# Kernel optimization log

Measured on AMD Instinct MI355X. Metric: run time of the kernel, lower is better.

## Reference

```python
import jax, jax.numpy as jnp
import numpy as np
from jax import lax

SR = 4096.0        # sample_rate_Hz
N_LAYERS = 4
N_STATE = 64       # state_dim
E = 2              # d_inner (expand=2, d_model=1)
K = 4              # depthwise conv kernel
DT_RANK = 1
B, L = 32, 4096


def setup_inputs() -> dict:
    key = jax.random.key(0)
    ks = jax.random.split(key, 10)
    s = 0.02
    x = jax.random.normal(ks[0], (B, L), dtype=jnp.float32)
    W_in   = jax.random.normal(ks[1], (N_LAYERS, 1, 2 * E), jnp.float32) * 1.0
    conv_w = jax.random.normal(ks[2], (N_LAYERS, E, K), jnp.float32) * 0.5
    conv_b = jnp.zeros((N_LAYERS, E), jnp.float32)
    W_x    = jax.random.normal(ks[3], (N_LAYERS, E, DT_RANK + 2 * N_STATE), jnp.float32) * s
    W_dt   = jax.random.normal(ks[4], (N_LAYERS, DT_RANK, E), jnp.float32) * s
    b_dt   = jnp.zeros((N_LAYERS, E), jnp.float32)
    # S4D-real style init: A = -exp(A_log), A_log = log(1..N)
    A_log  = jnp.broadcast_to(jnp.log(jnp.arange(1, N_STATE + 1, dtype=jnp.float32)), (N_LAYERS, E, N_STATE)).copy()
    D_skip = jnp.ones((N_LAYERS, E), jnp.float32)
    W_out  = jax.random.normal(ks[5], (N_LAYERS, E, 1), jnp.float32) * s
    return {"x": x, "W_in": W_in, "conv_w": conv_w, "conv_b": conv_b, "W_x": W_x,
            "W_dt": W_dt, "b_dt": b_dt, "A_log": A_log, "D_skip": D_skip, "W_out": W_out}


def _causal_dwconv(u, w, b):
    # u: [B,L,E], w: [E,K] depthwise causal conv
    Klen = w.shape[1]
    up = jnp.pad(u, ((0, 0), (Klen - 1, 0), (0, 0)))
    y = sum(up[:, k:k + u.shape[1], :] * w[None, None, :, k] for k in range(Klen))
    return y + b


def _selective_scan(u, delta, A, Bm, Cm, Dv):
    # u,delta: [B,L,E]; A: [E,N]; Bm,Cm: [B,L,N]; Dv: [E]
    dA = jnp.exp(delta[..., None] * A)                       # [B,L,E,N]
    dBu = delta[..., None] * Bm[:, :, None, :] * u[..., None]  # [B,L,E,N]

    def step(h, inp):
        dA_t, dBu_t, C_t = inp                               # [B,E,N],[B,E,N],[B,N]
        h = dA_t * h + dBu_t
        y = jnp.einsum('ben,bn->be', h, C_t)
        return h, y

    h0 = jnp.zeros((u.shape[0],) + A.shape, dtype=u.dtype)
    _, ys = lax.scan(step, h0, (dA.transpose(1, 0, 2, 3), dBu.transpose(1, 0, 2, 3), Cm.transpose(1, 0, 2)))
    return ys.transpose(1, 0, 2) + u * Dv                    # [B,L,E]


def _mamba_block(x, W_in, conv_w, conv_b, W_x, W_dt, b_dt, A_log, D_skip, W_out):
    # x: [B,L,1]
    xz = x @ W_in                                            # [B,L,2E]
    u, z = xz[..., :E], xz[..., E:]
    u = jax.nn.silu(_causal_dwconv(u, conv_w, conv_b))       # [B,L,E]
    proj = u @ W_x                                           # [B,L,DT_RANK+2N]
    dt = proj[..., :DT_RANK]
    Bm = proj[..., DT_RANK:DT_RANK + N_STATE]
    Cm = proj[..., DT_RANK + N_STATE:]
    delta = jax.nn.softplus(dt @ W_dt + b_dt) / SR           # [B,L,E], timestep tied to sample rate
    A = -jnp.exp(A_log)                                      # [E,N]
    y = _selective_scan(u, delta, A, Bm, Cm, D_skip)
    y = y * jax.nn.silu(z)
    return y @ W_out + x                                     # residual, [B,L,1]


def reference(x, W_in, conv_w, conv_b, W_x, W_dt, b_dt, A_log, D_skip, W_out):
    h = x[..., None]                                         # [B,L,1]
    for i in range(N_LAYERS):
        h = _mamba_block(h, W_in[i], conv_w[i], conv_b[i], W_x[i], W_dt[i],
                         b_dt[i], A_log[i], D_skip[i], W_out[i])
    return h[..., 0]
```

## Files before the change

### kernel.cpp

```cpp
#include <hip/hip_runtime.h>
#include <hip/hip_bf16.h>


constexpr int   Bsz = 32;
constexpr int   Lsz = 4096;
constexpr int   NC  = 64;
constexpr int   CL  = 64;
constexpr float SRinv = 1.0f / 4096.0f;

__device__ __forceinline__ float sigmoidf_(float v) {
    return 1.0f / (1.0f + __expf(-v));
}

__global__ __launch_bounds__(128) void k_chunk_scan(
    const float* __restrict__ xin,
    const float* __restrict__ W_in,
    const float* __restrict__ conv_w,
    const float* __restrict__ conv_b,
    const float* __restrict__ W_x,
    const float* __restrict__ W_dt,
    const float* __restrict__ b_dt,
    const float* __restrict__ A_log,
    float4* __restrict__ ud,
    float*  __restrict__ Pc,
    float*  __restrict__ Sc)
{
    const int c = blockIdx.x, b = blockIdx.y, tid = threadIdx.x;
    __shared__ float  xs[CL + 3];
    __shared__ float4 s_ud[CL];
    const int base = b * Lsz + c * CL;

    if (tid < CL + 3) {
        int l = c * CL + tid - 3;
        xs[tid] = (l >= 0) ? xin[b * Lsz + l] : 0.0f;
    }
    __syncthreads();

    if (tid < CL) {
        const int t = tid;
        float x0 = xs[t], x1 = xs[t + 1], x2 = xs[t + 2], x3 = xs[t + 3];
        float u[2];
        #pragma unroll
        for (int e = 0; e < 2; e++) {
            float v = W_in[e] * (x0 * conv_w[e * 4 + 0] + x1 * conv_w[e * 4 + 1] +
                                 x2 * conv_w[e * 4 + 2] + x3 * conv_w[e * 4 + 3]) +
                      conv_b[e];
            u[e] = v * sigmoidf_(v);
        }
        float dt = u[0] * W_x[0] + u[1] * W_x[129];
        float dl[2];
        #pragma unroll
        for (int e = 0; e < 2; e++) {
            float a = dt * W_dt[e] + b_dt[e];
            float sp = (a > 20.0f) ? a : log1pf(__expf(a));
            dl[e] = sp * SRinv;
        }
        float4 v4 = make_float4(u[0], u[1], dl[0], dl[1]);
        s_ud[t] = v4;
        ud[base + t] = v4;
    }
    __syncthreads();

    const int e = tid >> 6, n = tid & 63;
    const float Aen = -__expf(A_log[e * 64 + n]);
    const float wb0 = W_x[1 + n], wb1 = W_x[129 + 1 + n];
    float P = 1.0f, S = 0.0f;
    #pragma unroll 8
    for (int l = 0; l < CL; l++) {
        float4 v = s_ud[l];
        float ue = e ? v.y : v.x;
        float d  = e ? v.w : v.z;
        float Bn = v.x * wb0 + v.y * wb1;
        float dA = __expf(d * Aen);
        S = dA * S + (d * ue) * Bn;
        P *= dA;
    }
    const int idx = (b * NC + c) * 128 + tid;
    Pc[idx] = P;
    Sc[idx] = S;
}

__global__ __launch_bounds__(128) void k_output(
    const float* __restrict__ xin,
    const float4* __restrict__ ud,
    const float* __restrict__ Pc,
    const float* __restrict__ Sc,
    const float* __restrict__ W_in,
    const float* __restrict__ W_x,
    const float* __restrict__ A_log,
    const float* __restrict__ D_skip,
    const float* __restrict__ W_out,
    float* __restrict__ out)
{
    const int c = blockIdx.x, b = blockIdx.y, tid = threadIdx.x;
    constexpr int T = 32;
    __shared__ float4 s_ud[CL];
    __shared__ float  xs[CL];
    __shared__ float  ps[T * 2 * 65];
    __shared__ float  ys[T * 2];
    const int base = b * Lsz + c * CL;

    if (tid < CL) {
        s_ud[tid] = ud[base + tid];
        xs[tid]   = xin[base + tid];
    }

    const int e = tid >> 6, n = tid & 63;
    const float Aen = -__expf(A_log[e * 64 + n]);
    const float wb0 = W_x[1 + n],  wb1 = W_x[129 + 1 + n];
    const float wc0 = W_x[65 + n], wc1 = W_x[129 + 65 + n];
    const float wz0 = W_in[2], wz1 = W_in[3];
    const float D0 = D_skip[0], D1 = D_skip[1];
    const float wo0 = W_out[0], wo1 = W_out[1];

    float h = 0.0f;
    if (c > 0) {
        const float* Pb = Pc + (size_t)b * NC * 128 + tid;
        const float* Sb = Sc + (size_t)b * NC * 128 + tid;
        float runS = 0.0f, runP = 1.0f;
        #pragma unroll 8
        for (int j = c - 1; j >= 0; --j) {
            float Sj = Sb[j * 128];
            float Pj = Pb[j * 128];
            runS = __fmaf_rn(runP, Sj, runS);
            runP *= Pj;
        }
        h = runS;
    }
    __syncthreads();

    for (int tile = 0; tile < CL / T; tile++) {
        #pragma unroll 8
        for (int t = 0; t < T; t++) {
            float4 v = s_ud[tile * T + t];
            float ue = e ? v.y : v.x;
            float d  = e ? v.w : v.z;
            float Bn = v.x * wb0 + v.y * wb1;
            float Cn = v.x * wc0 + v.y * wc1;
            float dA = __expf(d * Aen);
            h = dA * h + (d * ue) * Bn;
            ps[(t * 2 + e) * 65 + n] = h * Cn;
        }
        __syncthreads();
        if (tid < T * 2) {
            const int r = tid, t = r >> 1, re = r & 1;
            const float* row = &ps[r * 65];
            float a0 = 0, a1 = 0, a2 = 0, a3 = 0;
            #pragma unroll
            for (int j = 0; j < 64; j += 4) {
                a0 += row[j]; a1 += row[j + 1]; a2 += row[j + 2]; a3 += row[j + 3];
            }
            float4 v = s_ud[tile * T + t];
            float ue = re ? v.y : v.x;
            ys[r] = (a0 + a1) + (a2 + a3) + ue * (re ? D1 : D0);
        }
        __syncthreads();
        if (tid < T) {
            int l = tile * T + tid;
            float y0 = ys[tid * 2], y1 = ys[tid * 2 + 1];
            float xv = xs[l];
            float z0 = xv * wz0, z1 = xv * wz1;
            out[base + l] = y0 * (z0 * sigmoidf_(z0)) * wo0 +
                            y1 * (z1 * sigmoidf_(z1)) * wo1 + xv;
        }
        __syncthreads();
    }
}

extern "C" void kernel_launch(void* const* d_in, const int* in_sizes, int n_in,
                              void* d_out, int out_size, void* d_ws, size_t ws_size,
                              hipStream_t stream) {
    const float* x      = (const float*)d_in[0];
    const float* W_in   = (const float*)d_in[1];
    const float* conv_w = (const float*)d_in[2];
    const float* conv_b = (const float*)d_in[3];
    const float* W_x    = (const float*)d_in[4];
    const float* W_dt   = (const float*)d_in[5];
    const float* b_dt   = (const float*)d_in[6];
    const float* A_log  = (const float*)d_in[7];
    const float* D_skip = (const float*)d_in[8];
    const float* W_out  = (const float*)d_in[9];
    float* out = (float*)d_out;

    float* ws   = (float*)d_ws;
    float4* ud  = (float4*)ws;
    float* Pc   = ws + (size_t)Bsz * Lsz * 4;
    float* Sc   = Pc + (size_t)Bsz * NC * 128;
    float* buf0 = Sc + (size_t)Bsz * NC * 128;
    float* buf1 = buf0 + (size_t)Bsz * Lsz;

    const float* cur = x;
    for (int i = 0; i < 4; i++) {
        float* o = (i == 3) ? out : ((i & 1) ? buf1 : buf0);
        k_chunk_scan<<<dim3(NC, Bsz), 128, 0, stream>>>(
            cur, W_in + i * 4, conv_w + i * 8, conv_b + i * 2,
            W_x + i * 258, W_dt + i * 2, b_dt + i * 2, A_log + i * 128,
            ud, Pc, Sc);
        k_output<<<dim3(NC, Bsz), 128, 0, stream>>>(
            cur, ud, Pc, Sc, W_in + i * 4, W_x + i * 258,
            A_log + i * 128, D_skip + i * 2, W_out + i * 2, o);
        cur = o;
    }
}
```

Measured before the change: 171.6 us.

## Use one 64-thread wave per chunk, each thread scanning both channels with float2

Both kernels drop from 128 to 64 threads per block. Each thread now handles one state index n for both inner channels at once, using two-wide float vectors, and the per-chunk P/S carries are stored as float2 pairs. This shares the B/C projection and the ud loads across the two channels, and it lets all 64 threads do the row reduction and the final output instead of idle subsets. The cost is half as many threads in flight and a longer dependent chain per thread, which may reduce latency hiding. The output kernel also reads ud straight from global memory rather than staging it in LDS.

New measurement: 166.8 us. 1.03x faster.

```diff
diff --git a/kernel.cpp b/kernel.cpp
--- a/kernel.cpp
+++ b/kernel.cpp
@@ -1,5 +1,4 @@
 #include <hip/hip_runtime.h>
-#include <hip/hip_bf16.h>
 
 
 constexpr int   Bsz = 32;
@@ -8,11 +7,13 @@
 constexpr int   CL  = 64;
 constexpr float SRinv = 1.0f / 4096.0f;
 
+typedef float fx2 __attribute__((ext_vector_type(2)));
+
 __device__ __forceinline__ float sigmoidf_(float v) {
     return 1.0f / (1.0f + __expf(-v));
 }
 
-__global__ __launch_bounds__(128) void k_chunk_scan(
+__global__ __launch_bounds__(64) void k_chunk_scan(
     const float* __restrict__ xin,
     const float* __restrict__ W_in,
     const float* __restrict__ conv_w,
@@ -22,23 +23,20 @@
     const float* __restrict__ b_dt,
     const float* __restrict__ A_log,
     float4* __restrict__ ud,
-    float*  __restrict__ Pc,
-    float*  __restrict__ Sc)
+    fx2* __restrict__ Pc,
+    fx2* __restrict__ Sc)
 {
-    const int c = blockIdx.x, b = blockIdx.y, tid = threadIdx.x;
+    const int c = blockIdx.x, b = blockIdx.y, n = threadIdx.x;
     __shared__ float  xs[CL + 3];
     __shared__ float4 s_ud[CL];
     const int base = b * Lsz + c * CL;
 
-    if (tid < CL + 3) {
-        int l = c * CL + tid - 3;
-        xs[tid] = (l >= 0) ? xin[b * Lsz + l] : 0.0f;
-    }
+    xs[3 + n] = xin[base + n];
+    if (n < 3) xs[n] = (c > 0) ? xin[base - 3 + n] : 0.0f;
     __syncthreads();
 
-    if (tid < CL) {
-        const int t = tid;
-        float x0 = xs[t], x1 = xs[t + 1], x2 = xs[t + 2], x3 = xs[t + 3];
+    {
+        float x0 = xs[n], x1 = xs[n + 1], x2 = xs[n + 2], x3 = xs[n + 3];
         float u[2];
         #pragma unroll
         for (int e = 0; e < 2; e++) {
@@ -56,35 +54,35 @@
             dl[e] = sp * SRinv;
         }
         float4 v4 = make_float4(u[0], u[1], dl[0], dl[1]);
-        s_ud[t] = v4;
-        ud[base + t] = v4;
+        s_ud[n] = v4;
+        ud[base + n] = v4;
     }
     __syncthreads();
 
-    const int e = tid >> 6, n = tid & 63;
-    const float Aen = -__expf(A_log[e * 64 + n]);
+    const fx2 A2 = { -__expf(A_log[n]), -__expf(A_log[64 + n]) };
     const float wb0 = W_x[1 + n], wb1 = W_x[129 + 1 + n];
-    float P = 1.0f, S = 0.0f;
+    fx2 P = {1.0f, 1.0f}, S = {0.0f, 0.0f};
     #pragma unroll 8
     for (int l = 0; l < CL; l++) {
         float4 v = s_ud[l];
-        float ue = e ? v.y : v.x;
-        float d  = e ? v.w : v.z;
         float Bn = v.x * wb0 + v.y * wb1;
-        float dA = __expf(d * Aen);
-        S = dA * S + (d * ue) * Bn;
+        fx2 u = {v.x, v.y};
+        fx2 d = {v.z, v.w};
+        fx2 darg = d * A2;
+        fx2 dA = { __expf(darg.x), __expf(darg.y) };
+        S = dA * S + (d * u) * Bn;
         P *= dA;
     }
-    const int idx = (b * NC + c) * 128 + tid;
+    const int idx = (b * NC + c) * 64 + n;
     Pc[idx] = P;
     Sc[idx] = S;
 }
 
-__global__ __launch_bounds__(128) void k_output(
+__global__ __launch_bounds__(64) void k_output(
     const float* __restrict__ xin,
     const float4* __restrict__ ud,
-    const float* __restrict__ Pc,
-    const float* __restrict__ Sc,
+    const fx2* __restrict__ Pc,
+    const fx2* __restrict__ Sc,
     const float* __restrict__ W_in,
     const float* __restrict__ W_x,
     const float* __restrict__ A_log,
@@ -92,78 +90,72 @@
     const float* __restrict__ W_out,
     float* __restrict__ out)
 {
-    const int c = blockIdx.x, b = blockIdx.y, tid = threadIdx.x;
+    const int c = blockIdx.x, b = blockIdx.y, n = threadIdx.x;
     constexpr int T = 32;
-    __shared__ float4 s_ud[CL];
-    __shared__ float  xs[CL];
-    __shared__ float  ps[T * 2 * 65];
-    __shared__ float  ys[T * 2];
+    __shared__ float ps[2 * T][65];
+    __shared__ float ys[2 * CL];
     const int base = b * Lsz + c * CL;
 
-    if (tid < CL) {
-        s_ud[tid] = ud[base + tid];
-        xs[tid]   = xin[base + tid];
-    }
-
-    const int e = tid >> 6, n = tid & 63;
-    const float Aen = -__expf(A_log[e * 64 + n]);
+    const fx2 A2 = { -__expf(A_log[n]), -__expf(A_log[64 + n]) };
     const float wb0 = W_x[1 + n],  wb1 = W_x[129 + 1 + n];
     const float wc0 = W_x[65 + n], wc1 = W_x[129 + 65 + n];
-    const float wz0 = W_in[2], wz1 = W_in[3];
-    const float D0 = D_skip[0], D1 = D_skip[1];
-    const float wo0 = W_out[0], wo1 = W_out[1];
 
-    float h = 0.0f;
+    fx2 h = {0.0f, 0.0f};
     if (c > 0) {
-        const float* Pb = Pc + (size_t)b * NC * 128 + tid;
-        const float* Sb = Sc + (size_t)b * NC * 128 + tid;
-        float runS = 0.0f, runP = 1.0f;
+        const fx2* Pb = Pc + (size_t)b * NC * 64 + n;
+        const fx2* Sb = Sc + (size_t)b * NC * 64 + n;
+        fx2 runS = {0.0f, 0.0f}, runP = {1.0f, 1.0f};
         #pragma unroll 8
         for (int j = c - 1; j >= 0; --j) {
-            float Sj = Sb[j * 128];
-            float Pj = Pb[j * 128];
-            runS = __fmaf_rn(runP, Sj, runS);
+            fx2 Sj = Sb[j * 64];
+            fx2 Pj = Pb[j * 64];
+            runS = runP * Sj + runS;
             runP *= Pj;
         }
         h = runS;
     }
-    __syncthreads();
 
-    for (int tile = 0; tile < CL / T; tile++) {
+    for (int tile = 0; tile < CL / T; ++tile) {
         #pragma unroll 8
-        for (int t = 0; t < T; t++) {
-            float4 v = s_ud[tile * T + t];
-            float ue = e ? v.y : v.x;
-            float d  = e ? v.w : v.z;
+        for (int q = 0; q < T; q++) {
+            float4 v = ud[base + tile * T + q];
             float Bn = v.x * wb0 + v.y * wb1;
             float Cn = v.x * wc0 + v.y * wc1;
-            float dA = __expf(d * Aen);
-            h = dA * h + (d * ue) * Bn;
-            ps[(t * 2 + e) * 65 + n] = h * Cn;
+            fx2 u = {v.x, v.y};
+            fx2 d = {v.z, v.w};
+            fx2 darg = d * A2;
+            fx2 dA = { __expf(darg.x), __expf(darg.y) };
+            h = dA * h + (d * u) * Bn;
+            fx2 yc = h * Cn;
+            ps[q * 2 + 0][n] = yc.x;
+            ps[q * 2 + 1][n] = yc.y;
         }
         __syncthreads();
-        if (tid < T * 2) {
-            const int r = tid, t = r >> 1, re = r & 1;
-            const float* row = &ps[r * 65];
+        {
+            const int r = n, q = r >> 1, re = r & 1;
+            const int t = tile * T + q;
+            const float* row = ps[r];
             float a0 = 0, a1 = 0, a2 = 0, a3 = 0;
             #pragma unroll
             for (int j = 0; j < 64; j += 4) {
                 a0 += row[j]; a1 += row[j + 1]; a2 += row[j + 2]; a3 += row[j + 3];
             }
-            float4 v = s_ud[tile * T + t];
+            float4 v = ud[base + t];
             float ue = re ? v.y : v.x;
-            ys[r] = (a0 + a1) + (a2 + a3) + ue * (re ? D1 : D0);
+            float De = re ? D_skip[1] : D_skip[0];
+            ys[t * 2 + re] = (a0 + a1) + (a2 + a3) + ue * De;
         }
         __syncthreads();
-        if (tid < T) {
-            int l = tile * T + tid;
-            float y0 = ys[tid * 2], y1 = ys[tid * 2 + 1];
-            float xv = xs[l];
-            float z0 = xv * wz0, z1 = xv * wz1;
-            out[base + l] = y0 * (z0 * sigmoidf_(z0)) * wo0 +
-                            y1 * (z1 * sigmoidf_(z1)) * wo1 + xv;
-        }
-        __syncthreads();
+    }
+
+    {
+        const float wz0 = W_in[2], wz1 = W_in[3];
+        const float wo0 = W_out[0], wo1 = W_out[1];
+        float xv = xin[base + n];
+        float y0 = ys[2 * n], y1 = ys[2 * n + 1];
+        float z0 = xv * wz0, z1 = xv * wz1;
+        out[base + n] = y0 * (z0 * sigmoidf_(z0)) * wo0 +
+                        y1 * (z1 * sigmoidf_(z1)) * wo1 + xv;
     }
 }
 
@@ -184,19 +176,19 @@
 
     float* ws   = (float*)d_ws;
     float4* ud  = (float4*)ws;
-    float* Pc   = ws + (size_t)Bsz * Lsz * 4;
-    float* Sc   = Pc + (size_t)Bsz * NC * 128;
-    float* buf0 = Sc + (size_t)Bsz * NC * 128;
+    fx2* Pc     = (fx2*)(ws + (size_t)Bsz * Lsz * 4);
+    fx2* Sc     = Pc + (size_t)Bsz * NC * 64;
+    float* buf0 = (float*)(Sc + (size_t)Bsz * NC * 64);
     float* buf1 = buf0 + (size_t)Bsz * Lsz;
 
     const float* cur = x;
     for (int i = 0; i < 4; i++) {
         float* o = (i == 3) ? out : ((i & 1) ? buf1 : buf0);
-        k_chunk_scan<<<dim3(NC, Bsz), 128, 0, stream>>>(
+        k_chunk_scan<<<dim3(NC, Bsz), 64, 0, stream>>>(
             cur, W_in + i * 4, conv_w + i * 8, conv_b + i * 2,
             W_x + i * 258, W_dt + i * 2, b_dt + i * 2, A_log + i * 128,
             ud, Pc, Sc);
-        k_output<<<dim3(NC, Bsz), 128, 0, stream>>>(
+        k_output<<<dim3(NC, Bsz), 64, 0, stream>>>(
             cur, ud, Pc, Sc, W_in + i * 4, W_x + i * 258,
             A_log + i * 128, D_skip + i * 2, W_out + i * 2, o);
         cur = o;
```
